# Kernel tuning notes

Hardware: AMD Instinct MI355X
Metric: run time of the kernel (lower is better)

Reference implementation:

```python
import jax, jax.numpy as jnp
import numpy as np

B, C, H, W = 32, 64, 96, 96
RED = 8


def setup_inputs() -> dict:
    key = jax.random.key(0)
    k0, k1, k2 = jax.random.split(key, 3)
    x = jax.random.normal(k0, (B, C, H, W), dtype=jnp.float32)
    # 1x1 conv weights (squeezed to linear): conv1 C->C//RED, conv2 C//RED->C
    w1 = jax.random.normal(k1, (C // RED, C), dtype=jnp.float32) * (1.0 / np.sqrt(C))
    b1 = jnp.zeros((C // RED,), dtype=jnp.float32)
    w2 = jax.random.normal(k2, (C, C // RED), dtype=jnp.float32) * (1.0 / np.sqrt(C // RED))
    b2 = jnp.zeros((C,), dtype=jnp.float32)
    return {"x": x, "w1": w1, "b1": b1, "w2": w2, "b2": b2}


def reference(x, w1, b1, w2, b2):
    Bx, Cx, Hx, Wx = x.shape
    M = Hx * Wx
    # --- covariance pooling: x @ I_hat @ x^T == centered outer product / M ---
    xr = x.reshape(Bx, Cx, M)
    xc = xr - xr.mean(axis=-1, keepdims=True)
    cov = jnp.einsum('bcm,bdm->bcd', xc, xc) / M  # (B, C, C)
    # --- Newton-Schulz matrix sqrt, iteration = 5 ---
    I3 = 3.0 * jnp.eye(Cx, dtype=x.dtype)  # broadcast over batch
    normA = jnp.trace(cov, axis1=1, axis2=2)  # (1/3 * cov * 3I).sum == trace
    A = cov / normA[:, None, None]
    ZY = 0.5 * (I3 - A)
    Y = A @ ZY
    Z = ZY
    for _ in range(3):  # range(1, iteration-1) with iteration=5
        ZY = (0.5 * (I3 - Z)) @ Y
        Y = Y @ ZY
        Z = ZY @ Z
    ZY = 0.5 * (Y @ (I3 - Z @ Y))
    cov_sqrt = ZY * jnp.sqrt(normA)[:, None, None]  # (B, C, C)
    # --- channel gating ---
    s = cov_sqrt.mean(axis=1)  # mean over dim=1 -> (B, C)
    h = jax.nn.relu(s @ w1.T + b1)
    gate = jax.nn.sigmoid(h @ w2.T + b2)  # (B, C)
    return x * gate[:, :, None, None]
```

## Files before the change

kernel.cpp:

```cpp
#include <hip/hip_runtime.h>
#include <math.h>


#define BB 32
#define CC 64
#define MM 9216

typedef __attribute__((ext_vector_type(8))) short bf16x8;
typedef __attribute__((ext_vector_type(4))) float f32x4;

__device__ __forceinline__ short f2bf(float f) {
  unsigned u = __builtin_bit_cast(unsigned, f);
  return (short)(unsigned short)((u + 0x8000u) >> 16);
}
__device__ __forceinline__ float bf2f(short h) {
  unsigned u = ((unsigned)(unsigned short)h) << 16;
  return __builtin_bit_cast(float, u);
}
__device__ __forceinline__ unsigned pack2(float lo, float hi) {
  unsigned ul = __builtin_bit_cast(unsigned, lo);
  unsigned uh = __builtin_bit_cast(unsigned, hi);
  return (uh & 0xffff0000u) | (ul >> 16);
}

#define NCHUNK 24
#define CHUNK_M (MM / NCHUNK)
#define WAVE_M (CHUNK_M / 4)
#define NSTEP (WAVE_M / 32)

__global__ __launch_bounds__(256, 3) void gram_k(const float* __restrict__ x,
                                                 float* __restrict__ covpart,
                                                 float* __restrict__ sumpart) {
  int b = blockIdx.x / NCHUNK;
  int chunk = blockIdx.x % NCHUNK;
  int tid = threadIdx.x;
  int w = tid >> 6, lane = tid & 63;
  int quad = lane >> 4, col = lane & 15;
  const float* xb = x + (size_t)b * CC * MM;
  int mwave = chunk * CHUNK_M + w * WAVE_M;

  f32x4 acc[4][4];
#pragma unroll
  for (int i = 0; i < 4; i++)
#pragma unroll
    for (int j = 0; j < 4; j++) acc[i][j] = (f32x4){0.f, 0.f, 0.f, 0.f};
  float csum[4] = {0.f, 0.f, 0.f, 0.f};

  const float* base[4];
#pragma unroll
  for (int rb = 0; rb < 4; rb++)
    base[rb] = xb + (size_t)(rb * 16 + col) * MM + mwave + quad * 8;

  float4 cur[4][2];
#pragma unroll
  for (int rb = 0; rb < 4; rb++) {
    cur[rb][0] = *(const float4*)(base[rb]);
    cur[rb][1] = *(const float4*)(base[rb] + 4);
  }
#pragma unroll
  for (int s = 0; s < NSTEP; s++) {
    float4 nxt[4][2];
    if (s + 1 < NSTEP) {
#pragma unroll
      for (int rb = 0; rb < 4; rb++) {
        const float* p = base[rb] + (s + 1) * 32;
        nxt[rb][0] = *(const float4*)(p);
        nxt[rb][1] = *(const float4*)(p + 4);
      }
    }
    bf16x8 frag[4];
#pragma unroll
    for (int rb = 0; rb < 4; rb++) {
      float v0 = cur[rb][0].x, v1 = cur[rb][0].y, v2 = cur[rb][0].z, v3 = cur[rb][0].w;
      float v4 = cur[rb][1].x, v5 = cur[rb][1].y, v6 = cur[rb][1].z, v7 = cur[rb][1].w;
      csum[rb] += ((v0 + v1) + (v2 + v3)) + ((v4 + v5) + (v6 + v7));
      bf16x8 f;
      unsigned* fu = (unsigned*)&f;
      fu[0] = pack2(v0, v1);
      fu[1] = pack2(v2, v3);
      fu[2] = pack2(v4, v5);
      fu[3] = pack2(v6, v7);
      frag[rb] = f;
    }
#pragma unroll
    for (int i = 0; i < 4; i++)
#pragma unroll
      for (int j = 0; j < 4; j++)
        acc[i][j] = __builtin_amdgcn_mfma_f32_16x16x32_bf16(frag[i], frag[j],
                                                            acc[i][j], 0, 0, 0);
    if (s + 1 < NSTEP) {
#pragma unroll
      for (int rb = 0; rb < 4; rb++) {
        cur[rb][0] = nxt[rb][0];
        cur[rb][1] = nxt[rb][1];
      }
    }
  }

  __shared__ float red[2][4096];
  __shared__ float swave[4][64];
  if (w >= 2) {
#pragma unroll
    for (int i = 0; i < 4; i++)
#pragma unroll
      for (int j = 0; j < 4; j++)
#pragma unroll
        for (int r = 0; r < 4; r++)
          red[w - 2][(i * 16 + quad * 4 + r) * 64 + j * 16 + col] = acc[i][j][r];
  }
#pragma unroll
  for (int rb = 0; rb < 4; rb++) {
    float c0 = csum[rb];
    c0 += __shfl_xor(c0, 16);
    c0 += __shfl_xor(c0, 32);
    if (lane < 16) swave[w][rb * 16 + lane] = c0;
  }
  __syncthreads();
  if (w < 2) {
#pragma unroll
    for (int i = 0; i < 4; i++)
#pragma unroll
      for (int j = 0; j < 4; j++)
#pragma unroll
        for (int r = 0; r < 4; r++)
          red[w][(i * 16 + quad * 4 + r) * 64 + j * 16 + col] += acc[i][j][r];
  }
  __syncthreads();
  float4* cp = (float4*)(covpart + (size_t)(b * NCHUNK + chunk) * 4096);
  const float4* r0 = (const float4*)red[0];
  const float4* r1 = (const float4*)red[1];
#pragma unroll
  for (int e = 0; e < 4; e++) {
    int idx = tid + 256 * e;
    float4 a = r0[idx], bb = r1[idx];
    a.x += bb.x; a.y += bb.y; a.z += bb.z; a.w += bb.w;
    cp[idx] = a;
  }
  if (tid < 64)
    sumpart[(size_t)(b * NCHUNK + chunk) * 64 + tid] =
        ((swave[0][tid] + swave[1][tid]) + (swave[2][tid] + swave[3][tid]));
}

__device__ __forceinline__ void mm64(short* __restrict__ D, const short* __restrict__ A,
                                     const short* __restrict__ Bm, int tid) {
  int w = tid >> 6, lane = tid & 63, quad = lane >> 4, col = lane & 15;
  f32x4 acc[4];
#pragma unroll
  for (int j = 0; j < 4; j++) acc[j] = (f32x4){0.f, 0.f, 0.f, 0.f};
#pragma unroll
  for (int ks = 0; ks < 2; ks++) {
    int k0 = ks * 32 + quad * 8;
    bf16x8 fa = *(const bf16x8*)(A + (w * 16 + col) * 64 + k0);
#pragma unroll
    for (int j = 0; j < 4; j++) {
      bf16x8 fb = *(const bf16x8*)(Bm + (j * 16 + col) * 64 + k0);
      acc[j] = __builtin_amdgcn_mfma_f32_16x16x32_bf16(fa, fb, acc[j], 0, 0, 0);
    }
  }
#pragma unroll
  for (int j = 0; j < 4; j++)
#pragma unroll
    for (int r = 0; r < 4; r++)
      D[(w * 16 + quad * 4 + r) * 64 + j * 16 + col] = f2bf(acc[j][r]);
}

__device__ __forceinline__ void mmcolsum(const short* __restrict__ A,
                                         const short* __restrict__ Bm,
                                         float* scol, int tid) {
  int w = tid >> 6, lane = tid & 63, quad = lane >> 4, col = lane & 15;
  f32x4 acc[4];
#pragma unroll
  for (int j = 0; j < 4; j++) acc[j] = (f32x4){0.f, 0.f, 0.f, 0.f};
#pragma unroll
  for (int ks = 0; ks < 2; ks++) {
    int k0 = ks * 32 + quad * 8;
    bf16x8 fa = *(const bf16x8*)(A + (w * 16 + col) * 64 + k0);
#pragma unroll
    for (int j = 0; j < 4; j++) {
      bf16x8 fb = *(const bf16x8*)(Bm + (j * 16 + col) * 64 + k0);
      acc[j] = __builtin_amdgcn_mfma_f32_16x16x32_bf16(fa, fb, acc[j], 0, 0, 0);
    }
  }
#pragma unroll
  for (int j = 0; j < 4; j++) {
    float t = (acc[j][0] + acc[j][1]) + (acc[j][2] + acc[j][3]);
    atomicAdd(&scol[j * 16 + col], t);
  }
}

__global__ __launch_bounds__(256) void ns_k(const float* __restrict__ covpart,
                                            const float* __restrict__ sumpart,
                                            const float* __restrict__ w1,
                                            const float* __restrict__ pb1,
                                            const float* __restrict__ w2,
                                            const float* __restrict__ pb2,
                                            float* __restrict__ gatews) {
  __shared__ __align__(16) short nb0[4096], nb1[4096], nb2[4096], nb3[4096], nb4[4096];
  __shared__ __align__(16) float gbuf[4096];
  __shared__ float mu[64];
  __shared__ float scol[64];
  __shared__ float hbuf[8];
  __shared__ float normA_sh;
  int b = blockIdx.x;
  int tid = threadIdx.x;

  const float4* cp = (const float4*)covpart + (size_t)b * NCHUNK * 1024;
  float4* gb4 = (float4*)gbuf;
#pragma unroll
  for (int e = 0; e < 4; e++) {
    int idx = tid + 256 * e;
    float4 s = {0.f, 0.f, 0.f, 0.f};
    for (int ch = 0; ch < NCHUNK; ch++) {
      float4 v = cp[(size_t)ch * 1024 + idx];
      s.x += v.x; s.y += v.y; s.z += v.z; s.w += v.w;
    }
    gb4[idx] = s;
  }
  if (tid < 64) {
    float s = 0.f;
    for (int ch = 0; ch < NCHUNK; ch++) s += sumpart[(size_t)(b * NCHUNK + ch) * 64 + tid];
    mu[tid] = s * (1.0f / MM);
  }
  __syncthreads();
  if (tid < 64) {
    float d = gbuf[tid * 65] * (1.0f / MM) - mu[tid] * mu[tid];
#pragma unroll
    for (int off = 32; off >= 1; off >>= 1) d += __shfl_down(d, off);
    if (tid == 0) normA_sh = d;
  }
  __syncthreads();
  float rn = 1.0f / normA_sh;
#pragma unroll
  for (int e = 0; e < 16; e++) {
    int idx = tid + 256 * e;
    int r = idx >> 6, c = idx & 63;
    float cv = gbuf[idx] * (1.0f / MM) - mu[r] * mu[c];
    float a = cv * rn;
    nb0[idx] = f2bf(a);
    nb1[idx] = f2bf((r == c ? 1.5f : 0.0f) - 0.5f * a);
  }
  __syncthreads();
  mm64(nb2, nb0, nb1, tid);
  __syncthreads();
  short *pY = nb2, *pZ = nb1, *s0 = nb3, *s1 = nb4, *s2 = nb0;
  for (int it = 0; it < 3; ++it) {
#pragma unroll
    for (int e = 0; e < 16; e++) {
      int idx = tid + 256 * e;
      int r = idx >> 6, c = idx & 63;
      float z = bf2f(pZ[idx]);
      s0[idx] = f2bf((r == c ? 1.5f : 0.0f) - 0.5f * z);
    }
    __syncthreads();
    mm64(s1, s0, pY, tid);
    __syncthreads();
    mm64(s2, pY, s1, tid);
    mm64(s0, s1, pZ, tid);
    __syncthreads();
    short* oY = pY; short* oZ = pZ; short* oW = s1;
    pY = s2; pZ = s0; s0 = oY; s1 = oZ; s2 = oW;
  }
  mm64(s0, pZ, pY, tid);
  __syncthreads();
#pragma unroll
  for (int e = 0; e < 16; e++) {
    int idx = tid + 256 * e;
    int r = idx >> 6, c = idx & 63;
    float p = bf2f(s0[idx]);
    s0[idx] = f2bf((r == c ? 3.0f : 0.0f) - p);
  }
  if (tid < 64) scol[tid] = 0.0f;
  __syncthreads();
  mmcolsum(pY, s0, scol, tid);
  __syncthreads();
  if (tid < 8) {
    float sc = 0.5f * sqrtf(normA_sh) * (1.0f / 64.0f);
    float acc = pb1[tid];
    for (int c = 0; c < 64; c++) acc += scol[c] * sc * w1[tid * 64 + c];
    hbuf[tid] = fmaxf(acc, 0.0f);
  }
  __syncthreads();
  if (tid < 64) {
    float acc = pb2[tid];
#pragma unroll
    for (int j = 0; j < 8; j++) acc += hbuf[j] * w2[tid * 8 + j];
    gatews[b * 64 + tid] = 1.0f / (1.0f + __expf(-acc));
  }
}

#define N4 (BB * CC * MM / 4)
__global__ __launch_bounds__(256) void gate_mul(const float* __restrict__ x,
                                                const float* __restrict__ gatews,
                                                float* __restrict__ out) {
  int i = blockIdx.x * 256 + threadIdx.x;
  int bc = i / 2304;
  float g = gatews[bc];
  float4 v = ((const float4*)x)[i];
  v.x *= g; v.y *= g; v.z *= g; v.w *= g;
  ((float4*)out)[i] = v;
}

extern "C" void kernel_launch(void* const* d_in, const int* in_sizes, int n_in,
                              void* d_out, int out_size, void* d_ws, size_t ws_size,
                              hipStream_t stream) {
  const float* x = (const float*)d_in[0];
  const float* w1 = (const float*)d_in[1];
  const float* b1 = (const float*)d_in[2];
  const float* w2 = (const float*)d_in[3];
  const float* b2 = (const float*)d_in[4];
  float* out = (float*)d_out;
  float* ws = (float*)d_ws;
  float* covpart = ws;
  float* sumpart = covpart + (size_t)BB * NCHUNK * 4096;
  float* gatews = sumpart + (size_t)BB * NCHUNK * 64;

  gram_k<<<BB * NCHUNK, 256, 0, stream>>>(x, covpart, sumpart);
  ns_k<<<BB, 256, 0, stream>>>(covpart, sumpart, w1, b1, w2, b2, gatews);
  gate_mul<<<N4 / 256, 256, 0, stream>>>(x, gatews, out);
}
```

Measured before the change: 192.5 us.

## Stage Gram tiles in swizzled shared memory and split output rows across waves

The covariance kernel now loads each 64x128 input tile cooperatively with coalesced float4 reads, converts it to bf16 and stores it into a double-buffered, XOR-swizzled shared-memory layout. Each wave computes one 16-row stripe of the Gram matrix from shared memory, which eliminates the cross-wave shared-memory reduction and lowers accumulator register count. Partial covariance and the final gated output are written with nontemporal stores. The cost is extra block-wide barriers per tile and shared-memory traffic for fragments.

```diff
diff --git a/kernel.cpp b/kernel.cpp
--- a/kernel.cpp
+++ b/kernel.cpp
@@ -5,6 +5,10 @@
 #define BB 32
 #define CC 64
 #define MM 9216
+
+#define MT 128
+#define NCHUNK 24
+#define TPB 3
 
 typedef __attribute__((ext_vector_type(8))) short bf16x8;
 typedef __attribute__((ext_vector_type(4))) float f32x4;
@@ -23,122 +27,108 @@
   return (uh & 0xffff0000u) | (ul >> 16);
 }
 
-#define NCHUNK 24
-#define CHUNK_M (MM / NCHUNK)
-#define WAVE_M (CHUNK_M / 4)
-#define NSTEP (WAVE_M / 32)
+__device__ __forceinline__ int gpos(int ch, int g) {
+  return ((ch >> 4) * 4 + (g >> 2)) * 64 + (g & 3) * 16 + ((ch & 15) ^ g);
+}
 
 __global__ __launch_bounds__(256, 3) void gram_k(const float* __restrict__ x,
                                                  float* __restrict__ covpart,
                                                  float* __restrict__ sumpart) {
+  __shared__ __align__(16) char smem[32768];
+  short* bufs[2] = {(short*)smem, (short*)(smem + 16384)};
+
   int b = blockIdx.x / NCHUNK;
   int chunk = blockIdx.x % NCHUNK;
   int tid = threadIdx.x;
   int w = tid >> 6, lane = tid & 63;
   int quad = lane >> 4, col = lane & 15;
   const float* xb = x + (size_t)b * CC * MM;
-  int mwave = chunk * CHUNK_M + w * WAVE_M;
-
-  f32x4 acc[4][4];
-#pragma unroll
-  for (int i = 0; i < 4; i++)
-#pragma unroll
-    for (int j = 0; j < 4; j++) acc[i][j] = (f32x4){0.f, 0.f, 0.f, 0.f};
-  float csum[4] = {0.f, 0.f, 0.f, 0.f};
-
-  const float* base[4];
-#pragma unroll
-  for (int rb = 0; rb < 4; rb++)
-    base[rb] = xb + (size_t)(rb * 16 + col) * MM + mwave + quad * 8;
-
-  float4 cur[4][2];
-#pragma unroll
-  for (int rb = 0; rb < 4; rb++) {
-    cur[rb][0] = *(const float4*)(base[rb]);
-    cur[rb][1] = *(const float4*)(base[rb] + 4);
-  }
-#pragma unroll
-  for (int s = 0; s < NSTEP; s++) {
-    float4 nxt[4][2];
-    if (s + 1 < NSTEP) {
-#pragma unroll
-      for (int rb = 0; rb < 4; rb++) {
-        const float* p = base[rb] + (s + 1) * 32;
-        nxt[rb][0] = *(const float4*)(p);
-        nxt[rb][1] = *(const float4*)(p + 4);
+  int mchunk = chunk * (MT * TPB);
+
+  f32x4 acc[4];
+#pragma unroll
+  for (int j = 0; j < 4; j++) acc[j] = (f32x4){0.f, 0.f, 0.f, 0.f};
+  float csum[8];
+#pragma unroll
+  for (int i = 0; i < 8; i++) csum[i] = 0.f;
+
+  int ch0 = tid >> 5;
+  int f4c = tid & 31;
+
+  float4 pre[8];
+#pragma unroll
+  for (int i = 0; i < 8; i++)
+    pre[i] = *(const float4*)(xb + (size_t)(ch0 + 8 * i) * MM + mchunk + f4c * 4);
+
+  {
+    int g = f4c >> 1, h = f4c & 1;
+#pragma unroll
+    for (int i = 0; i < 8; i++) {
+      float4 v = pre[i];
+      csum[i] += ((v.x + v.y) + (v.z + v.w));
+      uint2 d;
+      d.x = pack2(v.x, v.y);
+      d.y = pack2(v.z, v.w);
+      *(uint2*)((char*)bufs[0] + gpos(ch0 + 8 * i, g) * 16 + h * 8) = d;
+    }
+  }
+  __syncthreads();
+
+  for (int tl = 0; tl < TPB; ++tl) {
+    float4 nxt[8];
+    if (tl + 1 < TPB) {
+      int m0 = mchunk + (tl + 1) * MT;
+#pragma unroll
+      for (int i = 0; i < 8; i++)
+        nxt[i] = *(const float4*)(xb + (size_t)(ch0 + 8 * i) * MM + m0 + f4c * 4);
+    }
+    const short* buf = bufs[tl & 1];
+#pragma unroll
+    for (int ks = 0; ks < 4; ks++) {
+      int g = (ks << 2) | quad;
+      bf16x8 fr[4];
+#pragma unroll
+      for (int j = 0; j < 4; j++)
+        fr[j] = *(const bf16x8*)((const char*)buf +
+                                 ((j * 4 + ks) * 64 + quad * 16 + (col ^ g)) * 16);
+#pragma unroll
+      for (int j = 0; j < 4; j++)
+        acc[j] = __builtin_amdgcn_mfma_f32_16x16x32_bf16(fr[w], fr[j], acc[j], 0, 0, 0);
+    }
+    if (tl + 1 < TPB) {
+      short* nb = bufs[(tl + 1) & 1];
+      int g = f4c >> 1, h = f4c & 1;
+#pragma unroll
+      for (int i = 0; i < 8; i++) {
+        float4 v = nxt[i];
+        csum[i] += ((v.x + v.y) + (v.z + v.w));
+        uint2 d;
+        d.x = pack2(v.x, v.y);
+        d.y = pack2(v.z, v.w);
+        *(uint2*)((char*)nb + gpos(ch0 + 8 * i, g) * 16 + h * 8) = d;
       }
     }
-    bf16x8 frag[4];
-#pragma unroll
-    for (int rb = 0; rb < 4; rb++) {
-      float v0 = cur[rb][0].x, v1 = cur[rb][0].y, v2 = cur[rb][0].z, v3 = cur[rb][0].w;
-      float v4 = cur[rb][1].x, v5 = cur[rb][1].y, v6 = cur[rb][1].z, v7 = cur[rb][1].w;
-      csum[rb] += ((v0 + v1) + (v2 + v3)) + ((v4 + v5) + (v6 + v7));
-      bf16x8 f;
-      unsigned* fu = (unsigned*)&f;
-      fu[0] = pack2(v0, v1);
-      fu[1] = pack2(v2, v3);
-      fu[2] = pack2(v4, v5);
-      fu[3] = pack2(v6, v7);
-      frag[rb] = f;
-    }
-#pragma unroll
-    for (int i = 0; i < 4; i++)
-#pragma unroll
-      for (int j = 0; j < 4; j++)
-        acc[i][j] = __builtin_amdgcn_mfma_f32_16x16x32_bf16(frag[i], frag[j],
-                                                            acc[i][j], 0, 0, 0);
-    if (s + 1 < NSTEP) {
-#pragma unroll
-      for (int rb = 0; rb < 4; rb++) {
-        cur[rb][0] = nxt[rb][0];
-        cur[rb][1] = nxt[rb][1];
-      }
-    }
-  }
-
-  __shared__ float red[2][4096];
-  __shared__ float swave[4][64];
-  if (w >= 2) {
-#pragma unroll
-    for (int i = 0; i < 4; i++)
-#pragma unroll
-      for (int j = 0; j < 4; j++)
-#pragma unroll
-        for (int r = 0; r < 4; r++)
-          red[w - 2][(i * 16 + quad * 4 + r) * 64 + j * 16 + col] = acc[i][j][r];
-  }
-#pragma unroll
-  for (int rb = 0; rb < 4; rb++) {
-    float c0 = csum[rb];
-    c0 += __shfl_xor(c0, 16);
-    c0 += __shfl_xor(c0, 32);
-    if (lane < 16) swave[w][rb * 16 + lane] = c0;
-  }
-  __syncthreads();
-  if (w < 2) {
-#pragma unroll
-    for (int i = 0; i < 4; i++)
-#pragma unroll
-      for (int j = 0; j < 4; j++)
-#pragma unroll
-        for (int r = 0; r < 4; r++)
-          red[w][(i * 16 + quad * 4 + r) * 64 + j * 16 + col] += acc[i][j][r];
-  }
-  __syncthreads();
-  float4* cp = (float4*)(covpart + (size_t)(b * NCHUNK + chunk) * 4096);
-  const float4* r0 = (const float4*)red[0];
-  const float4* r1 = (const float4*)red[1];
-#pragma unroll
-  for (int e = 0; e < 4; e++) {
-    int idx = tid + 256 * e;
-    float4 a = r0[idx], bb = r1[idx];
-    a.x += bb.x; a.y += bb.y; a.z += bb.z; a.w += bb.w;
-    cp[idx] = a;
-  }
-  if (tid < 64)
-    sumpart[(size_t)(b * NCHUNK + chunk) * 64 + tid] =
-        ((swave[0][tid] + swave[1][tid]) + (swave[2][tid] + swave[3][tid]));
+    __syncthreads();
+  }
+
+  float* cp = covpart + (size_t)(b * NCHUNK + chunk) * 4096;
+#pragma unroll
+  for (int j = 0; j < 4; j++)
+#pragma unroll
+    for (int r = 0; r < 4; r++)
+      __builtin_nontemporal_store(acc[j][r],
+          cp + (w * 16 + quad * 4 + r) * 64 + j * 16 + col);
+
+  float* csl = (float*)smem;
+#pragma unroll
+  for (int i = 0; i < 8; i++) csl[(ch0 + 8 * i) * 32 + (tid & 31)] = csum[i];
+  __syncthreads();
+  if (tid < 64) {
+    float s = 0.f;
+#pragma unroll
+    for (int k = 0; k < 32; k++) s += csl[tid * 32 + k];
+    sumpart[(size_t)(b * NCHUNK + chunk) * 64 + tid] = s;
+  }
 }
 
 __device__ __forceinline__ void mm64(short* __restrict__ D, const short* __restrict__ A,
@@ -295,9 +285,9 @@
   int i = blockIdx.x * 256 + threadIdx.x;
   int bc = i / 2304;
   float g = gatews[bc];
-  float4 v = ((const float4*)x)[i];
-  v.x *= g; v.y *= g; v.z *= g; v.w *= g;
-  ((float4*)out)[i] = v;
+  f32x4 v = *(const f32x4*)((const float*)x + (size_t)i * 4);
+  v *= g;
+  __builtin_nontemporal_store(v, (f32x4*)((float*)out + (size_t)i * 4));
 }
 
 extern "C" void kernel_launch(void* const* d_in, const int* in_sizes, int n_in,
```

Result: slower. 215.7 us (+12.0%).
